# Kernel tuning notes

Measured on AMD Instinct MI355X. Metric: run time of the kernel, lower is better.

Reference implementation:

```python
import jax, jax.numpy as jnp
import numpy as np

N = 100000   # nodes
E = 1600000  # edges
D = 128      # in_dim
H = 128      # hidden_dim
G = 128      # graphs in batch


def setup_inputs() -> dict:
    key = jax.random.key(0)
    ks = jax.random.split(key, 16)
    inp = {
        "x": jax.random.normal(ks[0], (N, D), dtype=jnp.float32),
        "edge_index": jax.random.randint(ks[1], (2, E), 0, N, dtype=jnp.int32),
        "batch": jnp.sort(jax.random.randint(ks[2], (N,), 0, G, dtype=jnp.int32)),
    }
    dims = [(D, H), (H, H), (H, H)]
    k = 3
    for i, (di, dh) in enumerate(dims):
        inp[f"W1_{i}"] = jax.random.normal(ks[k], (di, dh), jnp.float32) * 0.05; k += 1
        inp[f"b1_{i}"] = jnp.zeros((dh,), jnp.float32)
        inp[f"W2_{i}"] = jax.random.normal(ks[k], (dh, dh), jnp.float32) * 0.05; k += 1
        inp[f"b2_{i}"] = jnp.zeros((dh,), jnp.float32)
    return inp


def _gin_layer(x, edge_index, W1, b1, W2, b2):
    # GINConv, eps=0: h_i = MLP(x_i + sum_{j->i} x_j)
    src, dst = edge_index[0], edge_index[1]
    agg = jax.ops.segment_sum(x[src], dst, num_segments=N)  # [N, d]
    h = x + agg
    h = jnp.maximum(h @ W1 + b1, 0.0)  # dropout = identity (eval)
    return h @ W2 + b2


def reference(x, edge_index, batch,
              W1_0, b1_0, W2_0, b2_0,
              W1_1, b1_1, W2_1, b2_1,
              W1_2, b1_2, W2_2, b2_2):
    params = [(W1_0, b1_0, W2_0, b2_0),
              (W1_1, b1_1, W2_1, b2_1),
              (W1_2, b1_2, W2_2, b2_2)]
    h = x
    for (W1, b1, W2, b2) in params:
        h = _gin_layer(h, edge_index, W1, b1, W2, b2)
    # global_mean_pool over batch indices
    sums = jax.ops.segment_sum(h, batch, num_segments=G)             # [G, H]
    cnts = jax.ops.segment_sum(jnp.ones((N,), h.dtype), batch, num_segments=G)
    return sums / jnp.maximum(cnts, 1.0)[:, None]
```

## Files before the change

### kernel.cpp

```cpp
#include <hip/hip_runtime.h>
#include <stdint.h>

#define NN 100000
#define NE 1600000
#define DD 128
#define NG 128
#define NPX 12500

using f32x4  = __attribute__((ext_vector_type(4))) float;
using bf16x8 = __attribute__((ext_vector_type(8))) __bf16;

__device__ __forceinline__ unsigned short f2bf(float f) {
  unsigned int u = __builtin_bit_cast(unsigned int, f);
  u = (u + 0x7FFFu + ((u >> 16) & 1u)) >> 16;
  return (unsigned short)u;
}

__device__ __forceinline__ float2 bfu(unsigned int u) {
  float2 r;
  r.x = __builtin_bit_cast(float, u << 16);
  r.y = __builtin_bit_cast(float, u & 0xffff0000u);
  return r;
}

__device__ __forceinline__ void addu4(float* a, uint4 v) {
  float2 p0 = bfu(v.x), p1 = bfu(v.y), p2 = bfu(v.z), p3 = bfu(v.w);
  a[0] += p0.x; a[1] += p0.y; a[2] += p1.x; a[3] += p1.y;
  a[4] += p2.x; a[5] += p2.y; a[6] += p3.x; a[7] += p3.y;
}

union ABu { uint4 q; bf16x8 v; };

__global__ void k_count(const int* __restrict__ dst, int* __restrict__ deg) {
  int xcd = blockIdx.x & 7;
  int e = (blockIdx.x >> 3) * 256 + threadIdx.x;
  if (e >= NE) return;
  int d = dst[e];
  if ((unsigned)(d - xcd * NPX) < (unsigned)NPX) atomicAdd(&deg[d], 1);
}

__global__ __launch_bounds__(1024) void k_scan(const int* __restrict__ deg,
                                               int* __restrict__ rowptr) {
  __shared__ int wsum[16];
  const int tid = threadIdx.x, wid = tid >> 6, lane = tid & 63;
  int carry = 0;
  for (int base = 0; base <= NN; base += 4096) {
    int idx = base + tid * 4;
    int v0 = (idx + 0 < NN) ? deg[idx + 0] : 0;
    int v1 = (idx + 1 < NN) ? deg[idx + 1] : 0;
    int v2 = (idx + 2 < NN) ? deg[idx + 2] : 0;
    int v3 = (idx + 3 < NN) ? deg[idx + 3] : 0;
    int tsum = v0 + v1 + v2 + v3;
    int sc = tsum;
    #pragma unroll
    for (int off = 1; off < 64; off <<= 1) {
      int n = __shfl_up(sc, off);
      if (lane >= off) sc += n;
    }
    if (lane == 63) wsum[wid] = sc;
    __syncthreads();
    if (wid == 0 && lane < 16) {
      int w = wsum[lane];
      #pragma unroll
      for (int off = 1; off < 16; off <<= 1) {
        int n = __shfl_up(w, off);
        if (lane >= off) w += n;
      }
      wsum[lane] = w;
    }
    __syncthreads();
    int woff = (wid ? wsum[wid - 1] : 0) + carry;
    int total = wsum[15];
    int excl = woff + sc - tsum;
    if (idx     <= NN) rowptr[idx]     = excl;
    if (idx + 1 <= NN) rowptr[idx + 1] = excl + v0;
    if (idx + 2 <= NN) rowptr[idx + 2] = excl + v0 + v1;
    if (idx + 3 <= NN) rowptr[idx + 3] = excl + v0 + v1 + v2;
    __syncthreads();
    carry += total;
  }
}

__global__ void k_fill(const int* __restrict__ src, const int* __restrict__ dst,
                       const int* __restrict__ rowptr, int* __restrict__ cursor,
                       int* __restrict__ csr) {
  int xcd = blockIdx.x & 7;
  int e = (blockIdx.x >> 3) * 256 + threadIdx.x;
  if (e >= NE) return;
  int d = dst[e];
  if ((unsigned)(d - xcd * NPX) < (unsigned)NPX) {
    int pos = rowptr[d] + atomicAdd(&cursor[d], 1);
    csr[pos] = src[e];
  }
}

__global__ void k_wconv(const float* __restrict__ w0, const float* __restrict__ w1,
                        const float* __restrict__ w2, const float* __restrict__ w3,
                        const float* __restrict__ w4, const float* __restrict__ w5,
                        unsigned short* __restrict__ wt) {
  int idx = blockIdx.x * 256 + threadIdx.x;
  if (idx >= 6 * 16384) return;
  int m = idx >> 14, rem = idx & 16383;
  int n = rem >> 7, k = rem & 127;
  const float* W = (m == 0) ? w0 : (m == 1) ? w1 : (m == 2) ? w2
                 : (m == 3) ? w3 : (m == 4) ? w4 : w5;
  wt[idx] = f2bf(W[k * 128 + n]);
}

__global__ void k_xconv(const float* __restrict__ x, unsigned short* __restrict__ xb) {
  int i = blockIdx.x * 256 + threadIdx.x;
  if (i >= NN * DD / 4) return;
  float4 v = ((const float4*)x)[i];
  uint2 p;
  p.x = (unsigned int)f2bf(v.x) | ((unsigned int)f2bf(v.y) << 16);
  p.y = (unsigned int)f2bf(v.z) | ((unsigned int)f2bf(v.w) << 16);
  ((uint2*)xb)[i] = p;
}

__global__ __launch_bounds__(256) void k_gin(const unsigned short* __restrict__ hb,
                                             const int* __restrict__ rowptr,
                                             const int* __restrict__ csr,
                                             const unsigned short* __restrict__ w1t,
                                             const float* __restrict__ b1,
                                             const unsigned short* __restrict__ w2t,
                                             const float* __restrict__ b2,
                                             unsigned short* __restrict__ hout) {
  __shared__ unsigned short tl[64 * DD];
  const int wid  = threadIdx.x >> 6;
  const int lane = threadIdx.x & 63;
  const int r16  = lane & 15;
  const int kg   = lane >> 4;
  const int waveBase = blockIdx.x * 64 + wid * 16;
  unsigned short* wt_ = tl + (wid * 16) * DD;
  const uint4* h4 = (const uint4*)hb;

  #pragma unroll
  for (int it = 0; it < 4; ++it) {
    const int lrow = it * 4 + kg;
    const int node = waveBase + lrow;
    float acc[8] = {0.f,0.f,0.f,0.f,0.f,0.f,0.f,0.f};
    if (node < NN) {
      addu4(acc, h4[(size_t)node * 16 + r16]);
      int j = rowptr[node];
      const int je = rowptr[node + 1];
      for (; j + 1 < je; j += 2) {
        int s0 = csr[j], s1 = csr[j + 1];
        uint4 v0 = h4[(size_t)s0 * 16 + r16];
        uint4 v1 = h4[(size_t)s1 * 16 + r16];
        addu4(acc, v0); addu4(acc, v1);
      }
      if (j < je) addu4(acc, h4[(size_t)csr[j] * 16 + r16]);
    }
    uint4 p;
    p.x = (unsigned int)f2bf(acc[0]) | ((unsigned int)f2bf(acc[1]) << 16);
    p.y = (unsigned int)f2bf(acc[2]) | ((unsigned int)f2bf(acc[3]) << 16);
    p.z = (unsigned int)f2bf(acc[4]) | ((unsigned int)f2bf(acc[5]) << 16);
    p.w = (unsigned int)f2bf(acc[6]) | ((unsigned int)f2bf(acc[7]) << 16);
    *(uint4*)(wt_ + lrow * DD + ((r16 ^ (lrow & 7)) << 3)) = p;
  }

  f32x4 acc[8];
  #pragma unroll
  for (int nb = 0; nb < 8; ++nb) acc[nb] = (f32x4){0.f, 0.f, 0.f, 0.f};
  #pragma unroll
  for (int s = 0; s < 4; ++s) {
    ABu au;
    au.q = *(const uint4*)(wt_ + r16 * DD + ((((s << 2) + kg) ^ (r16 & 7)) << 3));
    #pragma unroll
    for (int nb = 0; nb < 8; ++nb) {
      ABu bu; bu.q = *(const uint4*)(w1t + (nb * 16 + r16) * DD + s * 32 + kg * 8);
      acc[nb] = __builtin_amdgcn_mfma_f32_16x16x32_bf16(au.v, bu.v, acc[nb], 0, 0, 0);
    }
  }
  #pragma unroll
  for (int nb = 0; nb < 8; ++nb) {
    int n = nb * 16 + r16;
    float bias = b1[n];
    #pragma unroll
    for (int reg = 0; reg < 4; ++reg) {
      int urow = (kg << 2) + reg;
      float v = acc[nb][reg] + bias;
      v = v > 0.f ? v : 0.f;
      wt_[urow * DD + ((((n >> 3) ^ (urow & 7)) << 3) | (n & 7))] = f2bf(v);
    }
  }

  #pragma unroll
  for (int nb = 0; nb < 8; ++nb) acc[nb] = (f32x4){0.f, 0.f, 0.f, 0.f};
  #pragma unroll
  for (int s = 0; s < 4; ++s) {
    ABu au;
    au.q = *(const uint4*)(wt_ + r16 * DD + ((((s << 2) + kg) ^ (r16 & 7)) << 3));
    #pragma unroll
    for (int nb = 0; nb < 8; ++nb) {
      ABu bu; bu.q = *(const uint4*)(w2t + (nb * 16 + r16) * DD + s * 32 + kg * 8);
      acc[nb] = __builtin_amdgcn_mfma_f32_16x16x32_bf16(au.v, bu.v, acc[nb], 0, 0, 0);
    }
  }
  #pragma unroll
  for (int reg = 0; reg < 4; ++reg) {
    int row = waveBase + (kg << 2) + reg;
    if (row < NN) {
      #pragma unroll
      for (int nb = 0; nb < 8; ++nb) {
        int n = nb * 16 + r16;
        hout[row * DD + n] = f2bf(acc[nb][reg] + b2[n]);
      }
    }
  }
}

__global__ __launch_bounds__(256) void k_pool(const unsigned short* __restrict__ hb,
                                              const int* __restrict__ batch,
                                              float* __restrict__ out) {
  const int g  = blockIdx.x;
  const int f2 = threadIdx.x & 63;
  const int rp = threadIdx.x >> 6;
  int lo = 0, hi = NN;
  while (lo < hi) { int m = (lo + hi) >> 1; if (batch[m] < g) lo = m + 1; else hi = m; }
  const int start = lo;
  hi = NN;
  while (lo < hi) { int m = (lo + hi) >> 1; if (batch[m] < g + 1) lo = m + 1; else hi = m; }
  const int end = lo;

  const unsigned int* h32 = (const unsigned int*)hb;
  float2 acc = {0.f, 0.f};
  int i = start + rp;
  for (; i + 4 < end; i += 8) {
    float2 a = bfu(h32[(size_t)i * 64 + f2]);
    float2 b = bfu(h32[(size_t)(i + 4) * 64 + f2]);
    acc.x += a.x + b.x; acc.y += a.y + b.y;
  }
  for (; i < end; i += 4) {
    float2 a = bfu(h32[(size_t)i * 64 + f2]);
    acc.x += a.x; acc.y += a.y;
  }

  __shared__ float2 part[4][64];
  part[rp][f2] = acc;
  __syncthreads();
  if (rp == 0) {
    float2 t0 = part[0][f2], t1 = part[1][f2], t2 = part[2][f2], t3 = part[3][f2];
    float inv = 1.0f / (float)max(end - start, 1);
    out[g * DD + 2 * f2]     = (t0.x + t1.x + t2.x + t3.x) * inv;
    out[g * DD + 2 * f2 + 1] = (t0.y + t1.y + t2.y + t3.y) * inv;
  }
}

extern "C" void kernel_launch(void* const* d_in, const int* in_sizes, int n_in,
                              void* d_out, int out_size, void* d_ws, size_t ws_size,
                              hipStream_t stream) {
  const float* x    = (const float*)d_in[0];
  const int* ei     = (const int*)d_in[1];
  const int* src    = ei;
  const int* dst    = ei + NE;
  const int* batch  = (const int*)d_in[2];

  char* ws = (char*)d_ws;
  size_t off = 0;
  auto alloc = [&](size_t bytes) { char* p = ws + off; off = (off + bytes + 255) & ~(size_t)255; return p; };

  int*  deg    = (int*)alloc(2 * NN * 4);
  int*  cursor = deg + NN;
  int*  rowptr = (int*)alloc((NN + 1) * 4);
  int*  csr    = (int*)alloc(NE * 4);
  unsigned short* wt = (unsigned short*)alloc(6 * 16384 * 2);
  unsigned short* xb = (unsigned short*)alloc((size_t)NN * DD * 2);
  unsigned short* hA = (unsigned short*)alloc((size_t)NN * DD * 2);
  unsigned short* hB = (unsigned short*)alloc((size_t)NN * DD * 2);

  hipMemsetAsync(deg, 0, 2 * NN * 4, stream);

  k_wconv<<<(6 * 16384 + 255) / 256, 256, 0, stream>>>(
      (const float*)d_in[3], (const float*)d_in[5],
      (const float*)d_in[7], (const float*)d_in[9],
      (const float*)d_in[11], (const float*)d_in[13], wt);
  k_xconv<<<(NN * DD / 4 + 255) / 256, 256, 0, stream>>>(x, xb);

  const int echunks = (NE + 255) / 256;
  k_count<<<8 * echunks, 256, 0, stream>>>(dst, deg);
  k_scan<<<1, 1024, 0, stream>>>(deg, rowptr);
  k_fill<<<8 * echunks, 256, 0, stream>>>(src, dst, rowptr, cursor, csr);

  const unsigned short* hin = xb;
  unsigned short* houts[3] = {hA, hB, hA};
  for (int l = 0; l < 3; ++l) {
    k_gin<<<(NN + 63) / 64, 256, 0, stream>>>(
        hin, rowptr, csr,
        wt + (2 * l) * 16384, (const float*)d_in[4 + 4 * l],
        wt + (2 * l + 1) * 16384, (const float*)d_in[6 + 4 * l], houts[l]);
    hin = houts[l];
  }

  k_pool<<<NG, 256, 0, stream>>>(hin, batch, (float*)d_out);
}
```

Baseline: 717.9 us.

## Parallelize CSR row-pointer scan across blocks and use single-wave GIN blocks

Replaces the single-block serial prefix scan with a three-stage multi-block scan (per-block scan, block-sum scan, offset add). The GIN kernel now launches one 64-thread wave per block handling 16 nodes, and the neighbor gather loop is unrolled by four for more outstanding loads. This removes a serialized scan and improves scheduling granularity and memory-level parallelism, at the cost of two extra launches and more, smaller blocks.

Result: faster. 625.1 us (-12.9%).

```diff
diff --git a/kernel.cpp b/kernel.cpp
--- a/kernel.cpp
+++ b/kernel.cpp
@@ -6,6 +6,7 @@
 #define DD 128
 #define NG 128
 #define NPX 12500
+#define NBS 25
 
 using f32x4  = __attribute__((ext_vector_type(4))) float;
 using bf16x8 = __attribute__((ext_vector_type(8))) __bf16;
@@ -39,46 +40,64 @@
   if ((unsigned)(d - xcd * NPX) < (unsigned)NPX) atomicAdd(&deg[d], 1);
 }
 
-__global__ __launch_bounds__(1024) void k_scan(const int* __restrict__ deg,
-                                               int* __restrict__ rowptr) {
+__global__ __launch_bounds__(1024) void k_scanA(const int* __restrict__ deg,
+                                                int* __restrict__ rowptr,
+                                                int* __restrict__ bsum) {
   __shared__ int wsum[16];
   const int tid = threadIdx.x, wid = tid >> 6, lane = tid & 63;
-  int carry = 0;
-  for (int base = 0; base <= NN; base += 4096) {
-    int idx = base + tid * 4;
-    int v0 = (idx + 0 < NN) ? deg[idx + 0] : 0;
-    int v1 = (idx + 1 < NN) ? deg[idx + 1] : 0;
-    int v2 = (idx + 2 < NN) ? deg[idx + 2] : 0;
-    int v3 = (idx + 3 < NN) ? deg[idx + 3] : 0;
-    int tsum = v0 + v1 + v2 + v3;
-    int sc = tsum;
+  int idx = blockIdx.x * 4096 + tid * 4;
+  int v0 = (idx + 0 < NN) ? deg[idx + 0] : 0;
+  int v1 = (idx + 1 < NN) ? deg[idx + 1] : 0;
+  int v2 = (idx + 2 < NN) ? deg[idx + 2] : 0;
+  int v3 = (idx + 3 < NN) ? deg[idx + 3] : 0;
+  int tsum = v0 + v1 + v2 + v3;
+  int sc = tsum;
+  #pragma unroll
+  for (int off = 1; off < 64; off <<= 1) {
+    int n = __shfl_up(sc, off);
+    if (lane >= off) sc += n;
+  }
+  if (lane == 63) wsum[wid] = sc;
+  __syncthreads();
+  if (wid == 0 && lane < 16) {
+    int w = wsum[lane];
     #pragma unroll
-    for (int off = 1; off < 64; off <<= 1) {
-      int n = __shfl_up(sc, off);
-      if (lane >= off) sc += n;
-    }
-    if (lane == 63) wsum[wid] = sc;
-    __syncthreads();
-    if (wid == 0 && lane < 16) {
-      int w = wsum[lane];
-      #pragma unroll
-      for (int off = 1; off < 16; off <<= 1) {
-        int n = __shfl_up(w, off);
-        if (lane >= off) w += n;
-      }
-      wsum[lane] = w;
-    }
-    __syncthreads();
-    int woff = (wid ? wsum[wid - 1] : 0) + carry;
-    int total = wsum[15];
-    int excl = woff + sc - tsum;
-    if (idx     <= NN) rowptr[idx]     = excl;
-    if (idx + 1 <= NN) rowptr[idx + 1] = excl + v0;
-    if (idx + 2 <= NN) rowptr[idx + 2] = excl + v0 + v1;
-    if (idx + 3 <= NN) rowptr[idx + 3] = excl + v0 + v1 + v2;
-    __syncthreads();
-    carry += total;
-  }
+    for (int off = 1; off < 16; off <<= 1) {
+      int n = __shfl_up(w, off);
+      if (lane >= off) w += n;
+    }
+    wsum[lane] = w;
+  }
+  __syncthreads();
+  int excl = (wid ? wsum[wid - 1] : 0) + sc - tsum;
+  if (idx     <= NN) rowptr[idx]     = excl;
+  if (idx + 1 <= NN) rowptr[idx + 1] = excl + v0;
+  if (idx + 2 <= NN) rowptr[idx + 2] = excl + v0 + v1;
+  if (idx + 3 <= NN) rowptr[idx + 3] = excl + v0 + v1 + v2;
+  if (tid == 0) bsum[blockIdx.x] = 0;
+  if (tid == 1023) bsum[blockIdx.x] = wsum[15];
+}
+
+__global__ void k_scanB(int* __restrict__ bsum) {
+  int lane = threadIdx.x & 63;
+  int v = (lane < NBS) ? bsum[lane] : 0;
+  int sc = v;
+  #pragma unroll
+  for (int off = 1; off < 64; off <<= 1) {
+    int n = __shfl_up(sc, off);
+    if (lane >= off) sc += n;
+  }
+  if (lane < NBS) bsum[lane] = sc - v;
+}
+
+__global__ __launch_bounds__(1024) void k_scanC(int* __restrict__ rowptr,
+                                                const int* __restrict__ bsum) {
+  int add = bsum[blockIdx.x];
+  int idx = blockIdx.x * 4096 + threadIdx.x * 4;
+  if (idx     <= NN) rowptr[idx]     += add;
+  if (idx + 1 <= NN) rowptr[idx + 1] += add;
+  if (idx + 2 <= NN) rowptr[idx + 2] += add;
+  if (idx + 3 <= NN) rowptr[idx + 3] += add;
 }
 
 __global__ void k_fill(const int* __restrict__ src, const int* __restrict__ dst,
@@ -117,21 +136,19 @@
   ((uint2*)xb)[i] = p;
 }
 
-__global__ __launch_bounds__(256) void k_gin(const unsigned short* __restrict__ hb,
-                                             const int* __restrict__ rowptr,
-                                             const int* __restrict__ csr,
-                                             const unsigned short* __restrict__ w1t,
-                                             const float* __restrict__ b1,
-                                             const unsigned short* __restrict__ w2t,
-                                             const float* __restrict__ b2,
-                                             unsigned short* __restrict__ hout) {
-  __shared__ unsigned short tl[64 * DD];
-  const int wid  = threadIdx.x >> 6;
-  const int lane = threadIdx.x & 63;
+__global__ __launch_bounds__(64) void k_gin(const unsigned short* __restrict__ hb,
+                                            const int* __restrict__ rowptr,
+                                            const int* __restrict__ csr,
+                                            const unsigned short* __restrict__ w1t,
+                                            const float* __restrict__ b1,
+                                            const unsigned short* __restrict__ w2t,
+                                            const float* __restrict__ b2,
+                                            unsigned short* __restrict__ hout) {
+  __shared__ unsigned short wt_[16 * DD];
+  const int lane = threadIdx.x;
   const int r16  = lane & 15;
   const int kg   = lane >> 4;
-  const int waveBase = blockIdx.x * 64 + wid * 16;
-  unsigned short* wt_ = tl + (wid * 16) * DD;
+  const int waveBase = blockIdx.x * 16;
   const uint4* h4 = (const uint4*)hb;
 
   #pragma unroll
@@ -143,13 +160,15 @@
       addu4(acc, h4[(size_t)node * 16 + r16]);
       int j = rowptr[node];
       const int je = rowptr[node + 1];
-      for (; j + 1 < je; j += 2) {
-        int s0 = csr[j], s1 = csr[j + 1];
+      for (; j + 3 < je; j += 4) {
+        int s0 = csr[j], s1 = csr[j + 1], s2 = csr[j + 2], s3 = csr[j + 3];
         uint4 v0 = h4[(size_t)s0 * 16 + r16];
         uint4 v1 = h4[(size_t)s1 * 16 + r16];
-        addu4(acc, v0); addu4(acc, v1);
+        uint4 v2 = h4[(size_t)s2 * 16 + r16];
+        uint4 v3 = h4[(size_t)s3 * 16 + r16];
+        addu4(acc, v0); addu4(acc, v1); addu4(acc, v2); addu4(acc, v3);
       }
-      if (j < je) addu4(acc, h4[(size_t)csr[j] * 16 + r16]);
+      for (; j < je; ++j) addu4(acc, h4[(size_t)csr[j] * 16 + r16]);
     }
     uint4 p;
     p.x = (unsigned int)f2bf(acc[0]) | ((unsigned int)f2bf(acc[1]) << 16);
@@ -263,6 +282,7 @@
   int*  deg    = (int*)alloc(2 * NN * 4);
   int*  cursor = deg + NN;
   int*  rowptr = (int*)alloc((NN + 1) * 4);
+  int*  bsum   = (int*)alloc(NBS * 4);
   int*  csr    = (int*)alloc(NE * 4);
   unsigned short* wt = (unsigned short*)alloc(6 * 16384 * 2);
   unsigned short* xb = (unsigned short*)alloc((size_t)NN * DD * 2);
@@ -279,13 +299,15 @@
 
   const int echunks = (NE + 255) / 256;
   k_count<<<8 * echunks, 256, 0, stream>>>(dst, deg);
-  k_scan<<<1, 1024, 0, stream>>>(deg, rowptr);
+  k_scanA<<<NBS, 1024, 0, stream>>>(deg, rowptr, bsum);
+  k_scanB<<<1, 64, 0, stream>>>(bsum);
+  k_scanC<<<NBS, 1024, 0, stream>>>(rowptr, bsum);
   k_fill<<<8 * echunks, 256, 0, stream>>>(src, dst, rowptr, cursor, csr);
 
   const unsigned short* hin = xb;
   unsigned short* houts[3] = {hA, hB, hA};
   for (int l = 0; l < 3; ++l) {
-    k_gin<<<(NN + 63) / 64, 256, 0, stream>>>(
+    k_gin<<<(NN + 15) / 16, 64, 0, stream>>>(
         hin, rowptr, csr,
         wt + (2 * l) * 16384, (const float*)d_in[4 + 4 * l],
         wt + (2 * l + 1) * 16384, (const float*)d_in[6 + 4 * l], houts[l]);
```
